# Kernel tuning notes

Measured on AMD Instinct MI355X. Metric: run time of the kernel, lower is better.

Reference implementation:

```python
import math
import jax, jax.numpy as jnp
import numpy as np

N = 256                      # 'n' from __init__
LMAX = 15
NSH = (LMAX + 1) ** 2        # number of SH coefficients = 256
A = 2 * N                    # alpha grid size
B = N - 4                    # beta grid size (linspace(0,pi,n)[2:-2])
K = 1024                     # fixed max number of peaks per projection (jit-compatible capacity)
THR = 2.0 * math.pi / N      # dedup distance threshold


def _rot_zyz(a, b, c):
    def rz(t):
        return np.array([[math.cos(t), -math.sin(t), 0.0],
                         [math.sin(t),  math.cos(t), 0.0],
                         [0.0, 0.0, 1.0]])
    def ry(t):
        return np.array([[math.cos(t), 0.0, math.sin(t)],
                         [0.0, 1.0, 0.0],
                         [-math.sin(t), 0.0, math.cos(t)]])
    return rz(a) @ ry(b) @ rz(c)


def _grid_xyz(R):
    a = np.linspace(0.0, 2.0 * math.pi, A)
    b = np.linspace(0.0, math.pi, N)[2:-2]
    AA, BB = np.meshgrid(a, b, indexing='ij')       # [A, B]
    xyz = np.stack([np.sin(BB) * np.cos(AA),
                    np.sin(BB) * np.sin(AA),
                    np.cos(BB)], axis=-1)            # [A, B, 3]
    return (xyz @ R.T).astype(np.float32)


def setup_inputs() -> dict:
    key = jax.random.key(0)
    k1, k2, k3 = jax.random.split(key, 3)
    signal = jax.random.normal(k1, (NSH,), dtype=jnp.float32)
    # Precomputed SH projection buffers (fixed tensors in the torch module);
    # random stand-ins preserve the exact compute pattern of the einsum.
    sh1 = jax.random.normal(k2, (NSH, A, B), dtype=jnp.float32) * 0.1
    sh2 = jax.random.normal(k3, (NSH, A, B), dtype=jnp.float32) * 0.1
    xyz1 = jnp.asarray(_grid_xyz(_rot_zyz(math.pi / 2, math.pi / 2, math.pi / 2)))
    xyz2 = jnp.asarray(_grid_xyz(np.eye(3)))
    return {"signal": signal, "sh1": sh1, "sh2": sh2, "xyz1": xyz1, "xyz2": xyz2}


def _detect_peaks(signal, sh, xyz):
    # f[a,b] = sum_i signal[i] * sh[i,a,b]   (memory-bound GEMV over the grid)
    f = jnp.einsum('i,iab->ab', signal, sh)                       # [A, B]
    # strict local maxima along beta (rows) and alpha (columns); interior only
    row = jnp.pad((f[:, 1:-1] > f[:, :-2]) & (f[:, 1:-1] > f[:, 2:]),
                  ((0, 0), (1, 1)))
    col = jnp.pad((f[1:-1, :] > f[:-2, :]) & (f[1:-1, :] > f[2:, :]),
                  ((1, 1), (0, 0)))
    mask = (row & col).reshape(-1)                                # [A*B]
    ff = f.reshape(-1)
    score = jnp.where(mask, ff, -jnp.inf)
    _, idx = jax.lax.top_k(score, K)                              # fixed-capacity peak set
    valid = jnp.take(mask, idx)
    radius = jnp.where(valid, jnp.take(ff, idx), 0.0)             # [K]
    peaks = jnp.where(valid[:, None],
                      jnp.take(xyz.reshape(-1, 3), idx, axis=0), 0.0)  # [K, 3]
    return peaks, radius, valid


def reference(signal, sh1, sh2, xyz1, xyz2):
    p1, r1, v1 = _detect_peaks(signal, sh1, xyz1)
    p2, r2, v2 = _detect_peaks(signal, sh2, xyz2)
    # suppress peaks1 that lie within THR of any valid peak2
    d = jnp.linalg.norm(p1[:, None, :] - p2[None, :, :], axis=-1)  # [K, K]
    close = (d < THR) & v1[:, None] & v2[None, :]
    keep1 = v1 & ~jnp.any(close, axis=1)
    peaks = jnp.concatenate([jnp.where(keep1[:, None], p1, 0.0), p2], axis=0)   # [2K, 3]
    radius = jnp.concatenate([jnp.where(keep1, r1, 0.0), r2], axis=0)           # [2K]
    valid = jnp.concatenate([keep1, v2], axis=0)                                 # [2K]
    return peaks, radius, valid
```

## Files before the change

### kernel.cpp

```cpp
#include <hip/hip_runtime.h>
#include <hip/hip_bf16.h>
#include <stdint.h>

#define NSH 256
#define AG 512
#define BG 252
#define AB (AG*BG)
#define KK 1024
#define SENT 0xFFFFFFFFFFFFFFFFull

static __device__ __forceinline__ unsigned int fkey(float v){
    unsigned int u = __float_as_uint(v);
    u ^= (u >> 31) ? 0xFFFFFFFFu : 0x80000000u;
    return u;
}

__global__ __launch_bounds__(256) void k_gemv(const float* __restrict__ sig,
        const float* __restrict__ sh1, const float* __restrict__ sh2,
        float* __restrict__ f, unsigned int* __restrict__ counts){
    if (blockIdx.x == 0 && blockIdx.y == 0 && threadIdx.x < 2)
        counts[threadIdx.x] = 0;
    int proj = blockIdx.y;
    const float* sh = proj ? sh2 : sh1;
    size_t j4 = ((size_t)blockIdx.x * 256 + threadIdx.x) * 4;
    const float* p = sh + j4;
    float a0 = 0.f, a1 = 0.f, a2 = 0.f, a3 = 0.f;
    float4 bufA[8], bufB[8];
    #pragma unroll
    for (int u = 0; u < 8; ++u)
        bufA[u] = *reinterpret_cast<const float4*>(p + (size_t)u * AB);
    #pragma unroll
    for (int ii = 0; ii < NSH; ii += 16){
        #pragma unroll
        for (int u = 0; u < 8; ++u){
            int nx = ii + 8 + u;
            if (nx < NSH) bufB[u] = *reinterpret_cast<const float4*>(p + (size_t)nx * AB);
        }
        #pragma unroll
        for (int u = 0; u < 8; ++u){
            float si = sig[ii + u];
            a0 = fmaf(si, bufA[u].x, a0);
            a1 = fmaf(si, bufA[u].y, a1);
            a2 = fmaf(si, bufA[u].z, a2);
            a3 = fmaf(si, bufA[u].w, a3);
        }
        #pragma unroll
        for (int u = 0; u < 8; ++u){
            int nx = ii + 16 + u;
            if (nx < NSH) bufA[u] = *reinterpret_cast<const float4*>(p + (size_t)nx * AB);
        }
        #pragma unroll
        for (int u = 0; u < 8; ++u){
            float si = sig[ii + 8 + u];
            a0 = fmaf(si, bufB[u].x, a0);
            a1 = fmaf(si, bufB[u].y, a1);
            a2 = fmaf(si, bufB[u].z, a2);
            a3 = fmaf(si, bufB[u].w, a3);
        }
    }
    float4 o; o.x = a0; o.y = a1; o.z = a2; o.w = a3;
    *reinterpret_cast<float4*>(f + (size_t)proj * AB + j4) = o;
}

__global__ __launch_bounds__(256) void k_mask(const float* __restrict__ f,
        unsigned long long* __restrict__ cand, unsigned int* __restrict__ counts){
    int proj = blockIdx.y;
    const float* fp = f + (size_t)proj * AB;
    int j = blockIdx.x * 256 + threadIdx.x;
    bool pred = false;
    unsigned long long key = 0;
    {
        int a = j / BG, b = j - a * BG;
        if (a > 0 && a < AG - 1 && b > 0 && b < BG - 1){
            float v = fp[j];
            pred = (v > fp[j-1]) && (v > fp[j+1]) && (v > fp[j-BG]) && (v > fp[j+BG]);
            if (pred)
                key = (((unsigned long long)(~fkey(v))) << 32) | (unsigned int)j;
        }
    }
    unsigned long long bal = __ballot(pred);
    if (bal){
        int lane = threadIdx.x & 63;
        int leader = __ffsll(bal) - 1;
        unsigned int base = 0;
        if (lane == leader) base = atomicAdd(&counts[proj], (unsigned int)__popcll(bal));
        base = __shfl(base, leader);
        if (pred){
            unsigned int off = (unsigned int)__popcll(bal & ((1ull << lane) - 1ull));
            cand[(size_t)proj * AB + base + off] = key;
        }
    }
}

__global__ __launch_bounds__(1024) void k_select(const unsigned long long* __restrict__ cand,
        const unsigned int* __restrict__ counts, unsigned long long* __restrict__ sel){
    int proj = blockIdx.y;
    const unsigned long long* cp = cand + (size_t)proj * AB;
    unsigned long long* sp = sel + proj * KK;
    unsigned int count = counts[proj];
    int tid = threadIdx.x;
    if (count <= KK){
        if (tid < KK) sp[tid] = SENT;
        if (tid < (int)count) sp[tid] = cp[tid];
        return;
    }
    __shared__ unsigned int hist[256];
    __shared__ unsigned int sbin, sremk;
    unsigned long long prefix = 0, pmask = 0;
    unsigned int remk = KK;
    for (int lvl = 7; lvl >= 0; --lvl){
        int shft = lvl * 8;
        if (tid < 256) hist[tid] = 0;
        __syncthreads();
        for (unsigned int i = tid; i < count; i += 1024){
            unsigned long long k = cp[i];
            if ((k & pmask) == prefix)
                atomicAdd(&hist[(unsigned int)(k >> shft) & 255u], 1u);
        }
        __syncthreads();
        if (tid < 64){
            unsigned int b0 = hist[tid*4+0], b1 = hist[tid*4+1];
            unsigned int b2 = hist[tid*4+2], b3 = hist[tid*4+3];
            unsigned int lsum = b0 + b1 + b2 + b3;
            unsigned int incl = lsum;
            #pragma unroll
            for (int off = 1; off < 64; off <<= 1){
                unsigned int v = __shfl_up(incl, off);
                if (tid >= off) incl += v;
            }
            unsigned int excl = incl - lsum;
            if (excl < remk && remk <= incl){
                unsigned int r = remk - excl;
                unsigned int c0 = b0, c01 = b0 + b1, c012 = b0 + b1 + b2;
                unsigned int bin, rr;
                if (r <= c0){ bin = tid*4+0; rr = r; }
                else if (r <= c01){ bin = tid*4+1; rr = r - c0; }
                else if (r <= c012){ bin = tid*4+2; rr = r - c01; }
                else { bin = tid*4+3; rr = r - c012; }
                sbin = bin; sremk = rr;
            }
        }
        __syncthreads();
        prefix |= ((unsigned long long)sbin) << shft;
        pmask  |= 0xFFull << shft;
        remk = sremk;
        __syncthreads();
    }
    __shared__ unsigned int pos;
    if (tid == 0) pos = 0;
    __syncthreads();
    for (unsigned int i = tid; i < count; i += 1024){
        unsigned long long k = cp[i];
        if (k <= prefix){
            unsigned int p = atomicAdd(&pos, 1u);
            sp[p] = k;
        }
    }
}

__global__ __launch_bounds__(1024) void k_sortgather(const unsigned long long* __restrict__ sel,
        const float* __restrict__ f, const float* __restrict__ xyz1,
        const float* __restrict__ xyz2, float4* __restrict__ pr,
        unsigned int* __restrict__ vb, float* __restrict__ out){
    int proj = blockIdx.y;
    int tid = threadIdx.x;
    __shared__ unsigned long long s[KK];
    s[tid] = sel[proj * KK + tid];
    __syncthreads();
    for (int k = 2; k <= KK; k <<= 1){
        for (int j = k >> 1; j > 0; j >>= 1){
            int ixj = tid ^ j;
            if (ixj > tid){
                unsigned long long a = s[tid], b = s[ixj];
                bool asc = (tid & k) == 0;
                if ((a > b) == asc){ s[tid] = b; s[ixj] = a; }
            }
            __syncthreads();
        }
    }
    unsigned long long key = s[tid];
    bool val = (key != SENT);
    unsigned int j = (unsigned int)key;
    const float* fp = f + (size_t)proj * AB;
    const float* xyz = proj ? xyz2 : xyz1;
    float4 o = make_float4(0.f, 0.f, 0.f, 0.f);
    if (val){
        o.x = xyz[(size_t)j * 3 + 0];
        o.y = xyz[(size_t)j * 3 + 1];
        o.z = xyz[(size_t)j * 3 + 2];
        o.w = fp[j];
    }
    pr[proj * KK + tid] = o;
    vb[proj * KK + tid] = val ? 1u : 0u;
    if (proj == 1){
        int row = KK + tid;
        out[row * 3 + 0] = o.x;
        out[row * 3 + 1] = o.y;
        out[row * 3 + 2] = o.z;
        out[2 * KK * 3 + row] = o.w;
        out[2 * KK * 3 + 2 * KK + row] = val ? 1.0f : 0.0f;
    }
}

__global__ __launch_bounds__(256) void k_dedup(const float4* __restrict__ pr,
        const unsigned int* __restrict__ vb, float* __restrict__ out){
    const float THRF = (float)(6.283185307179586 / 256.0);
    int tid = threadIdx.x;
    __shared__ float sx[KK], sy[KK], sz[KK];
    #pragma unroll
    for (int t = 0; t < 4; ++t){
        int idx = t * 256 + tid;
        float4 v = pr[KK + idx];
        bool v2 = vb[KK + idx] != 0;
        sx[idx] = v2 ? v.x : 1e9f;
        sy[idx] = v2 ? v.y : 1e9f;
        sz[idx] = v2 ? v.z : 1e9f;
    }
    __syncthreads();
    int k = blockIdx.x * 256 + tid;
    float4 m = pr[k];
    bool close = false;
    {
        #pragma clang fp contract(off)
        #pragma unroll 8
        for (int jj = 0; jj < KK; ++jj){
            float dx = m.x - sx[jj];
            float dy = m.y - sy[jj];
            float dz = m.z - sz[jj];
            float d2 = dx * dx + dy * dy + dz * dz;
            close = close | (sqrtf(d2) < THRF);
        }
    }
    bool keep = (vb[k] != 0) && !close;
    out[k * 3 + 0] = keep ? m.x : 0.0f;
    out[k * 3 + 1] = keep ? m.y : 0.0f;
    out[k * 3 + 2] = keep ? m.z : 0.0f;
    out[2 * KK * 3 + k] = keep ? m.w : 0.0f;
    out[2 * KK * 3 + 2 * KK + k] = keep ? 1.0f : 0.0f;
}

extern "C" void kernel_launch(void* const* d_in, const int* in_sizes, int n_in,
                              void* d_out, int out_size, void* d_ws, size_t ws_size,
                              hipStream_t stream){
    const float* sig  = (const float*)d_in[0];
    const float* sh1  = (const float*)d_in[1];
    const float* sh2  = (const float*)d_in[2];
    const float* xyz1 = (const float*)d_in[3];
    const float* xyz2 = (const float*)d_in[4];
    float* out = (float*)d_out;
    char* ws = (char*)d_ws;

    float* f                  = (float*)(ws);
    unsigned long long* cand  = (unsigned long long*)(ws + 0x100000);
    unsigned int* counts      = (unsigned int*)(ws + 0x300000);
    unsigned long long* sel   = (unsigned long long*)(ws + 0x300100);
    float4* pr                = (float4*)(ws + 0x310000);
    unsigned int* vb          = (unsigned int*)(ws + 0x320000);

    k_gemv<<<dim3(AB / 1024, 2), dim3(256), 0, stream>>>(sig, sh1, sh2, f, counts);
    k_mask<<<dim3(AB / 256, 2), dim3(256), 0, stream>>>(f, cand, counts);
    k_select<<<dim3(1, 2), dim3(1024), 0, stream>>>(cand, counts, sel);
    k_sortgather<<<dim3(1, 2), dim3(1024), 0, stream>>>(sel, f, xyz1, xyz2, pr, vb, out);
    k_dedup<<<dim3(4, 1), dim3(256), 0, stream>>>(pr, vb, out);
}
```

Measured before the change: 213.2 us.

## Stream GEMV rows through LDS with async global_load_lds ring buffer

Replaces the register double-buffered float4 loads in the SH GEMV kernel with a 16-deep LDS ring buffer. Each wave fills its own slice of the buffer using global_load_lds direct-to-LDS loads, and a manual s_waitcnt vmcnt throttle keeps 16 rows in flight per wave. The signal vector is also staged once in shared memory. The aim is deeper memory-level parallelism on this bandwidth-bound pass with fewer VGPRs. The cost is 64KB of LDS per block, which limits occupancy, and a dependence on hand-written wait-count ordering for correctness.

```diff
diff --git a/kernel.cpp b/kernel.cpp
--- a/kernel.cpp
+++ b/kernel.cpp
@@ -7,6 +7,7 @@
 #define BG 252
 #define AB (AG*BG)
 #define KK 1024
+#define DEPTH 16
 #define SENT 0xFFFFFFFFFFFFFFFFull
 
 static __device__ __forceinline__ unsigned int fkey(float v){
@@ -15,51 +16,42 @@
     return u;
 }
 
+#define GLOAD_LDS(gp, lp) __builtin_amdgcn_global_load_lds( \
+    (__attribute__((address_space(1))) void*)(gp), \
+    (__attribute__((address_space(3))) void*)(lp), 16, 0, 0)
+
 __global__ __launch_bounds__(256) void k_gemv(const float* __restrict__ sig,
         const float* __restrict__ sh1, const float* __restrict__ sh2,
         float* __restrict__ f, unsigned int* __restrict__ counts){
-    if (blockIdx.x == 0 && blockIdx.y == 0 && threadIdx.x < 2)
-        counts[threadIdx.x] = 0;
+    __shared__ float sig_s[NSH];
+    __shared__ float tile[DEPTH][1024];
+    int tid = threadIdx.x;
+    if (blockIdx.x == 0 && blockIdx.y == 0 && tid < 2) counts[tid] = 0;
+    sig_s[tid] = sig[tid];
+    __syncthreads();
     int proj = blockIdx.y;
     const float* sh = proj ? sh2 : sh1;
-    size_t j4 = ((size_t)blockIdx.x * 256 + threadIdx.x) * 4;
-    const float* p = sh + j4;
+    int jbase = blockIdx.x * 1024;
+    int wave = tid >> 6, lane = tid & 63;
+    int wslot = wave * 256 + lane * 4;
+    const float* gsrc = sh + jbase + wslot;
+    #pragma unroll
+    for (int ipf = 0; ipf < DEPTH; ++ipf)
+        GLOAD_LDS(gsrc + (size_t)ipf * AB, &tile[ipf][wave * 256]);
     float a0 = 0.f, a1 = 0.f, a2 = 0.f, a3 = 0.f;
-    float4 bufA[8], bufB[8];
-    #pragma unroll
-    for (int u = 0; u < 8; ++u)
-        bufA[u] = *reinterpret_cast<const float4*>(p + (size_t)u * AB);
-    #pragma unroll
-    for (int ii = 0; ii < NSH; ii += 16){
-        #pragma unroll
-        for (int u = 0; u < 8; ++u){
-            int nx = ii + 8 + u;
-            if (nx < NSH) bufB[u] = *reinterpret_cast<const float4*>(p + (size_t)nx * AB);
-        }
-        #pragma unroll
-        for (int u = 0; u < 8; ++u){
-            float si = sig[ii + u];
-            a0 = fmaf(si, bufA[u].x, a0);
-            a1 = fmaf(si, bufA[u].y, a1);
-            a2 = fmaf(si, bufA[u].z, a2);
-            a3 = fmaf(si, bufA[u].w, a3);
-        }
-        #pragma unroll
-        for (int u = 0; u < 8; ++u){
-            int nx = ii + 16 + u;
-            if (nx < NSH) bufA[u] = *reinterpret_cast<const float4*>(p + (size_t)nx * AB);
-        }
-        #pragma unroll
-        for (int u = 0; u < 8; ++u){
-            float si = sig[ii + 8 + u];
-            a0 = fmaf(si, bufB[u].x, a0);
-            a1 = fmaf(si, bufB[u].y, a1);
-            a2 = fmaf(si, bufB[u].z, a2);
-            a3 = fmaf(si, bufB[u].w, a3);
-        }
+    for (int i = 0; i < NSH; ++i){
+        asm volatile("s_waitcnt vmcnt(15)" ::: "memory");
+        float4 v = *reinterpret_cast<const float4*>(&tile[i & (DEPTH-1)][wslot]);
+        float si = sig_s[i];
+        int pf = i + DEPTH; pf = pf > NSH - 1 ? NSH - 1 : pf;
+        GLOAD_LDS(gsrc + (size_t)pf * AB, &tile[i & (DEPTH-1)][wave * 256]);
+        a0 = fmaf(si, v.x, a0);
+        a1 = fmaf(si, v.y, a1);
+        a2 = fmaf(si, v.z, a2);
+        a3 = fmaf(si, v.w, a3);
     }
     float4 o; o.x = a0; o.y = a1; o.z = a2; o.w = a3;
-    *reinterpret_cast<float4*>(f + (size_t)proj * AB + j4) = o;
+    *reinterpret_cast<float4*>(f + (size_t)proj * AB + jbase + wslot) = o;
 }
 
 __global__ __launch_bounds__(256) void k_mask(const float* __restrict__ f,
```

Result: slower. 252.2 us (+18.3%).
